# Optimization experiments

Measured on AMD Instinct MI355X. Metric: run time of the kernel, lower is better.

Reference implementation:

```python
import jax, jax.numpy as jnp
import numpy as np

N_NODES = 100000
N_EDGES = 1600000
IN_DIM = 128
HID_DIM = 64
OUT_DIM = 128
EPS = 1e-5


def setup_inputs() -> dict:
    key = jax.random.key(0)
    ks = jax.random.split(key, 10)
    feat = jax.random.normal(ks[0], (N_NODES, IN_DIM), dtype=jnp.float32)
    src = jax.random.randint(ks[1], (N_EDGES,), 0, N_NODES)
    dst = jax.random.randint(ks[2], (N_EDGES,), 0, N_NODES)
    # learned params
    gamma = jnp.ones((IN_DIM,), jnp.float32)
    beta = jnp.zeros((IN_DIM,), jnp.float32)
    Wq = jax.random.normal(ks[3], (IN_DIM, HID_DIM), jnp.float32) * 0.05
    bq = jax.random.normal(ks[4], (HID_DIM,), jnp.float32) * 0.05
    Wk = jax.random.normal(ks[5], (IN_DIM, HID_DIM), jnp.float32) * 0.05
    Wv = jax.random.normal(ks[6], (IN_DIM, OUT_DIM), jnp.float32) * 0.05
    We = jax.random.normal(ks[7], (HID_DIM, 1), jnp.float32) * 0.05
    return {"feat": feat, "src": src, "dst": dst, "gamma": gamma, "beta": beta,
            "Wq": Wq, "bq": bq, "Wk": Wk, "Wv": Wv, "We": We}


def reference(feat, src, dst, gamma, beta, Wq, bq, Wk, Wv, We):
    # BatchNorm1d (training-mode batch stats, biased variance)
    mean = jnp.mean(feat, axis=0)
    var = jnp.mean((feat - mean) ** 2, axis=0)
    x = (feat - mean) * jax.lax.rsqrt(var + EPS) * gamma + beta
    # feat_drop = 0.0 -> identity
    q = x @ Wq + bq          # [N, H]
    k = x @ Wk               # [N, H]
    v = x @ Wv               # [N, O]
    # u_add_v: src-node q + dst-node k per edge, then sigmoid and fc_e -> scalar score
    e = jax.nn.sigmoid(q[src] + k[dst]) @ We  # [E, 1]
    e = e[:, 0]                               # [E]
    # edge_softmax: softmax over incoming edges of each destination node
    m = jax.ops.segment_max(e, dst, num_segments=N_NODES)  # [N]
    ex = jnp.exp(e - m[dst])
    s = jax.ops.segment_sum(ex, dst, num_segments=N_NODES)  # [N]
    a = ex / s[dst]                                          # [E]
    # u_mul_e_sum: weighted scatter-sum of source v into destinations
    rst = jax.ops.segment_sum(v[src] * a[:, None], dst, num_segments=N_NODES)  # [N, O]
    return rst
```

## Files before the change

kernel.cpp:

```cpp
#include <hip/hip_runtime.h>
#include <math.h>

#define IN_DIM 128
#define HID 64
#define OUT_DIM 128
#define ELL_W 64
#define NPART 8
constexpr float EPS = 1e-5f;

typedef short short8 __attribute__((ext_vector_type(8)));
typedef float f32x4  __attribute__((ext_vector_type(4)));
typedef int   i32x4  __attribute__((ext_vector_type(4)));


__device__ inline ushort f2bf(float x) {
    __bf16 h = (__bf16)x;
    return *reinterpret_cast<ushort*>(&h);
}
__device__ inline short f2bfs(float x) {
    __bf16 h = (__bf16)x;
    return *reinterpret_cast<short*>(&h);
}
__device__ inline float bf2f(ushort u) {
    union { unsigned u; float f; } c; c.u = ((unsigned)u) << 16;
    return c.f;
}
__device__ inline float4 bf4_to_f4(ushort4 u) {
    return make_float4(bf2f(u.x), bf2f(u.y), bf2f(u.z), bf2f(u.w));
}

__global__ __launch_bounds__(256) void stats_kernel(
    const float* __restrict__ feat, float* __restrict__ ws, int n_nodes)
{
    int col  = threadIdx.x & 127;
    int half = threadIdx.x >> 7;
    float sum = 0.f, sq = 0.f;
    for (int r = blockIdx.x * 2 + half; r < n_nodes; r += gridDim.x * 2) {
        float x = feat[r * IN_DIM + col];
        sum += x; sq += x * x;
    }
    __shared__ float redS[256], redQ[256];
    redS[threadIdx.x] = sum; redQ[threadIdx.x] = sq;
    __syncthreads();
    if (threadIdx.x < 128) {
        sum = redS[threadIdx.x] + redS[threadIdx.x + 128];
        sq  = redQ[threadIdx.x] + redQ[threadIdx.x + 128];
        unsafeAtomicAdd(&ws[col], sum);
        unsafeAtomicAdd(&ws[128 + col], sq);
    }
}

__global__ __launch_bounds__(256) void wprep(
    const float* __restrict__ Wq, const float* __restrict__ Wk,
    const float* __restrict__ Wv, ushort* __restrict__ Bfrag)
{
    int gid  = blockIdx.x * 256 + threadIdx.x;
    int f    = gid >> 6;
    int lane = gid & 63;
    int kc = f & 3, ct = (f >> 2) & 3, w = f >> 4;
    int col   = w * 64 + ct * 16 + (lane & 15);
    int kbase = kc * 32 + (lane >> 4) * 8;
    ushort tmp[8];
    #pragma unroll
    for (int j = 0; j < 8; j++) {
        int k = kbase + j;
        float val;
        if (col < 64)       val = Wq[k * HID + col];
        else if (col < 128) val = Wk[k * HID + (col - 64)];
        else                val = Wv[k * OUT_DIM + (col - 128)];
        tmp[j] = f2bf(val);
    }
    ushort* d = &Bfrag[(f * 64 + lane) * 8];
    *(ushort4*)d       = make_ushort4(tmp[0], tmp[1], tmp[2], tmp[3]);
    *(ushort4*)(d + 4) = make_ushort4(tmp[4], tmp[5], tmp[6], tmp[7]);
}

__global__ __launch_bounds__(256) void mfma_qkv(
    const float* __restrict__ feat, const ushort* __restrict__ Bfrag,
    const float* __restrict__ bq,
    const float* __restrict__ gamma, const float* __restrict__ beta,
    const float* __restrict__ stats,
    ushort* __restrict__ qb, ushort* __restrict__ kb, ushort* __restrict__ vb,
    int n_nodes)
{
    __shared__ float sc[IN_DIM], sh[IN_DIM];
    int tid = threadIdx.x;
    if (tid < 128) {
        float inv_n = 1.0f / (float)n_nodes;
        float mean = stats[tid] * inv_n;
        float var  = stats[128 + tid] * inv_n - mean * mean;
        float s    = gamma[tid] * rsqrtf(var + EPS);
        sc[tid] = s; sh[tid] = beta[tid] - mean * s;
    }

    int w    = tid >> 6;
    int lane = tid & 63;
    int row0 = blockIdx.x * 64;
    int m    = lane & 15;
    int quad = lane >> 4;
    int nm1  = n_nodes - 1;

    short8 bfr[16];
    #pragma unroll
    for (int f = 0; f < 16; f++)
        bfr[f] = *(const short8*)&Bfrag[((w * 16 + f) * 64 + lane) * 8];

    __syncthreads();

    f32x4 acc[4][4] = {};

    #pragma unroll
    for (int kc = 0; kc < 4; kc++) {
        int koff = kc * 32 + quad * 8;
        float4 sc0 = *(const float4*)&sc[koff];
        float4 sc1 = *(const float4*)&sc[koff + 4];
        float4 sh0 = *(const float4*)&sh[koff];
        float4 sh1 = *(const float4*)&sh[koff + 4];
        short8 afr[4];
        #pragma unroll
        for (int rt = 0; rt < 4; rt++) {
            int row = row0 + rt * 16 + m;
            row = row < nm1 ? row : nm1;
            const float* fp = &feat[(size_t)row * IN_DIM + koff];
            float4 x0 = *(const float4*)fp;
            float4 x1 = *(const float4*)(fp + 4);
            afr[rt][0] = f2bfs(x0.x * sc0.x + sh0.x);
            afr[rt][1] = f2bfs(x0.y * sc0.y + sh0.y);
            afr[rt][2] = f2bfs(x0.z * sc0.z + sh0.z);
            afr[rt][3] = f2bfs(x0.w * sc0.w + sh0.w);
            afr[rt][4] = f2bfs(x1.x * sc1.x + sh1.x);
            afr[rt][5] = f2bfs(x1.y * sc1.y + sh1.y);
            afr[rt][6] = f2bfs(x1.z * sc1.z + sh1.z);
            afr[rt][7] = f2bfs(x1.w * sc1.w + sh1.w);
        }
        #pragma unroll
        for (int rt = 0; rt < 4; rt++)
            #pragma unroll
            for (int ct = 0; ct < 4; ct++)
                acc[rt][ct] = __builtin_amdgcn_mfma_f32_16x16x32_bf16(
                    afr[rt], bfr[ct * 4 + kc], acc[rt][ct], 0, 0, 0);
    }

    ushort* base; int ld, cl;
    if (w == 0)      { base = qb; ld = HID;     cl = 0; }
    else if (w == 1) { base = kb; ld = HID;     cl = 0; }
    else             { base = vb; ld = OUT_DIM; cl = (w - 2) * 64; }

    #pragma unroll
    for (int ct = 0; ct < 4; ct++) {
        int col = cl + ct * 16 + m;
        float bias = (w == 0) ? bq[ct * 16 + m] : 0.f;
        #pragma unroll
        for (int rt = 0; rt < 4; rt++) {
            int r0 = row0 + rt * 16 + quad * 4;
            #pragma unroll
            for (int r = 0; r < 4; r++)
                base[(size_t)(r0 + r) * ld + col] = f2bf(acc[rt][ct][r] + bias);
        }
    }
}

__global__ __launch_bounds__(256) void fill_ell_part(
    const int* __restrict__ src, const int* __restrict__ dst,
    int* __restrict__ deg, int* __restrict__ ell,
    int n_edges, int part_size)
{
    int p  = blockIdx.x & (NPART - 1);
    int gb = blockIdx.x >> 3;
    int nb = gridDim.x >> 3;
    unsigned lo = (unsigned)(p * part_size);
    unsigned ps = (unsigned)part_size;

    int idx    = gb * 256 + threadIdx.x;
    int stride = nb * 256;
    int n4     = n_edges >> 2;

    const i32x4* dst4 = reinterpret_cast<const i32x4*>(dst);
    const i32x4* src4 = reinterpret_cast<const i32x4*>(src);

    for (int i = idx; i < n4; i += stride) {
        i32x4 d4 = __builtin_nontemporal_load(dst4 + i);
        i32x4 s4 = __builtin_nontemporal_load(src4 + i);
        #pragma unroll
        for (int j = 0; j < 4; j++) {
            unsigned d = (unsigned)d4[j];
            if (d - lo < ps) {
                int pos = atomicAdd(&deg[d], 1);
                if (pos < ELL_W) ell[(size_t)d * ELL_W + pos] = s4[j];
            }
        }
    }
    for (int e = (n4 << 2) + idx; e < n_edges; e += stride) {
        unsigned d = (unsigned)dst[e];
        if (d - lo < ps) {
            int pos = atomicAdd(&deg[d], 1);
            if (pos < ELL_W) ell[(size_t)d * ELL_W + pos] = src[e];
        }
    }
}

__global__ __launch_bounds__(256) void hist_kernel(
    const int* __restrict__ dst, int* __restrict__ deg, int n_edges)
{
    int e = blockIdx.x * 256 + threadIdx.x;
    if (e < n_edges) atomicAdd(&deg[dst[e]], 1);
}

#define SCAN_B 256

__global__ __launch_bounds__(256) void scan_partial(
    const int* __restrict__ deg, int* __restrict__ part, int n)
{
    int chunk = (n + SCAN_B - 1) / SCAN_B;
    int lo = blockIdx.x * chunk;
    int hi = lo + chunk; if (hi > n) hi = n;
    int s = 0;
    for (int i = lo + threadIdx.x; i < hi; i += 256) s += deg[i];
    __shared__ int red[256];
    red[threadIdx.x] = s; __syncthreads();
    for (int d = 128; d; d >>= 1) {
        if (threadIdx.x < d) red[threadIdx.x] += red[threadIdx.x + d];
        __syncthreads();
    }
    if (threadIdx.x == 0) part[blockIdx.x] = red[0];
}

__global__ __launch_bounds__(256) void scan_combine(
    int* __restrict__ part, int* __restrict__ offsets, int n)
{
    __shared__ int tmp[256];
    int t = threadIdx.x;
    int v = part[t];
    tmp[t] = v; __syncthreads();
    for (int d = 1; d < 256; d <<= 1) {
        int cur = tmp[t];
        int add = (t >= d) ? tmp[t - d] : 0;
        __syncthreads();
        tmp[t] = cur + add;
        __syncthreads();
    }
    part[t] = tmp[t] - v;
    if (t == 255) offsets[n] = tmp[255];
}

__global__ __launch_bounds__(256) void scan_final(
    const int* __restrict__ deg, const int* __restrict__ part,
    int* __restrict__ offsets, int* __restrict__ cursor, int n)
{
    __shared__ int tmp[256];
    int t = threadIdx.x;
    int chunk = (n + SCAN_B - 1) / SCAN_B;
    int lo = blockIdx.x * chunk;
    int hi = lo + chunk; if (hi > n) hi = n;
    int base = part[blockIdx.x];
    for (int i0 = lo; i0 < hi; i0 += 256) {
        int i = i0 + t;
        int d = (i < hi) ? deg[i] : 0;
        tmp[t] = d; __syncthreads();
        for (int s = 1; s < 256; s <<= 1) {
            int cur = tmp[t];
            int add = (t >= s) ? tmp[t - s] : 0;
            __syncthreads();
            tmp[t] = cur + add;
            __syncthreads();
        }
        int excl = tmp[t] - d;
        int total = tmp[255];
        if (i < hi) { offsets[i] = base + excl; cursor[i] = base + excl; }
        base += total;
        __syncthreads();
    }
}

__global__ __launch_bounds__(256) void fill_kernel(
    const int* __restrict__ src, const int* __restrict__ dst,
    int* __restrict__ cursor, int* __restrict__ csr_src, int n_edges)
{
    int e = blockIdx.x * 256 + threadIdx.x;
    if (e < n_edges) {
        int d = dst[e];
        int pos = atomicAdd(&cursor[d], 1);
        csr_src[pos] = src[e];
    }
}

__device__ inline void gather_core(
    const int* __restrict__ row, int cnt, int node, int h, int sub,
    const ushort* __restrict__ qb, const ushort* __restrict__ kb,
    const ushort* __restrict__ vb, const float* __restrict__ We,
    float* __restrict__ out)
{
    if (cnt == 0) {
        if (sub == 0) {
            float4 z = make_float4(0.f, 0.f, 0.f, 0.f);
            *(float4*)&out[node * OUT_DIM + 4 * h]      = z;
            *(float4*)&out[node * OUT_DIM + 64 + 4 * h] = z;
        }
        return;
    }

    float4 kd = bf4_to_f4(*(const ushort4*)&kb[node * HID + 4 * h]);
    float4 we = *(const float4*)&We[4 * h];

    float4 o0 = make_float4(0.f, 0.f, 0.f, 0.f);
    float4 o1 = make_float4(0.f, 0.f, 0.f, 0.f);
    float ssum = 0.f;

    for (int p0 = 0; p0 < cnt; p0 += 4) {
        int p = p0 + sub;
        bool act = (p < cnt);
        int sN = row[act ? p : 0];
        float4 qv = bf4_to_f4(*(const ushort4*)&qb[sN * HID + 4 * h]);
        float t;
        t  = we.x * __fdividef(1.f, 1.f + __expf(-(qv.x + kd.x)));
        t += we.y * __fdividef(1.f, 1.f + __expf(-(qv.y + kd.y)));
        t += we.z * __fdividef(1.f, 1.f + __expf(-(qv.z + kd.z)));
        t += we.w * __fdividef(1.f, 1.f + __expf(-(qv.w + kd.w)));
        t += __shfl_xor(t, 1);
        t += __shfl_xor(t, 2);
        t += __shfl_xor(t, 4);
        t += __shfl_xor(t, 8);
        float exv = act ? __expf(t) : 0.f;
        ssum += exv;
        float4 v0 = bf4_to_f4(*(const ushort4*)&vb[sN * OUT_DIM + 4 * h]);
        float4 v1 = bf4_to_f4(*(const ushort4*)&vb[sN * OUT_DIM + 64 + 4 * h]);
        o0.x += exv * v0.x; o0.y += exv * v0.y;
        o0.z += exv * v0.z; o0.w += exv * v0.w;
        o1.x += exv * v1.x; o1.y += exv * v1.y;
        o1.z += exv * v1.z; o1.w += exv * v1.w;
    }

    ssum += __shfl_xor(ssum, 16); ssum += __shfl_xor(ssum, 32);
    o0.x += __shfl_xor(o0.x, 16); o0.x += __shfl_xor(o0.x, 32);
    o0.y += __shfl_xor(o0.y, 16); o0.y += __shfl_xor(o0.y, 32);
    o0.z += __shfl_xor(o0.z, 16); o0.z += __shfl_xor(o0.z, 32);
    o0.w += __shfl_xor(o0.w, 16); o0.w += __shfl_xor(o0.w, 32);
    o1.x += __shfl_xor(o1.x, 16); o1.x += __shfl_xor(o1.x, 32);
    o1.y += __shfl_xor(o1.y, 16); o1.y += __shfl_xor(o1.y, 32);
    o1.z += __shfl_xor(o1.z, 16); o1.z += __shfl_xor(o1.z, 32);
    o1.w += __shfl_xor(o1.w, 16); o1.w += __shfl_xor(o1.w, 32);

    if (sub == 0) {
        float inv = (ssum > 0.f) ? __fdividef(1.f, ssum) : 0.f;
        o0.x *= inv; o0.y *= inv; o0.z *= inv; o0.w *= inv;
        o1.x *= inv; o1.y *= inv; o1.z *= inv; o1.w *= inv;
        *(float4*)&out[node * OUT_DIM + 4 * h]      = o0;
        *(float4*)&out[node * OUT_DIM + 64 + 4 * h] = o1;
    }
}

__global__ __launch_bounds__(256) void gather_ell(
    const int* __restrict__ deg, const int* __restrict__ ell,
    const ushort* __restrict__ qb, const ushort* __restrict__ kb,
    const ushort* __restrict__ vb, const float* __restrict__ We,
    float* __restrict__ out, int n_nodes)
{
    int node = (blockIdx.x * 256 + threadIdx.x) >> 6;
    int lane = threadIdx.x & 63;
    if (node >= n_nodes) return;
    int cnt = deg[node];
    cnt = cnt < ELL_W ? cnt : ELL_W;
    gather_core(&ell[(size_t)node * ELL_W], cnt, node,
                lane & 15, lane >> 4, qb, kb, vb, We, out);
}

__global__ __launch_bounds__(256) void gather_csr(
    const int* __restrict__ offsets, const int* __restrict__ csr_src,
    const ushort* __restrict__ qb, const ushort* __restrict__ kb,
    const ushort* __restrict__ vb, const float* __restrict__ We,
    float* __restrict__ out, int n_nodes)
{
    int node = (blockIdx.x * 256 + threadIdx.x) >> 6;
    int lane = threadIdx.x & 63;
    if (node >= n_nodes) return;
    int beg = offsets[node];
    int cnt = offsets[node + 1] - beg;
    gather_core(&csr_src[beg], cnt, node,
                lane & 15, lane >> 4, qb, kb, vb, We, out);
}

extern "C" void kernel_launch(void* const* d_in, const int* in_sizes, int n_in,
                              void* d_out, int out_size, void* d_ws, size_t ws_size,
                              hipStream_t stream)
{
    const float* feat  = (const float*)d_in[0];
    const int*   src   = (const int*)d_in[1];
    const int*   dst   = (const int*)d_in[2];
    const float* gamma = (const float*)d_in[3];
    const float* beta  = (const float*)d_in[4];
    const float* Wq    = (const float*)d_in[5];
    const float* bq    = (const float*)d_in[6];
    const float* Wk    = (const float*)d_in[7];
    const float* Wv    = (const float*)d_in[8];
    const float* We    = (const float*)d_in[9];

    int n_nodes = in_sizes[0] / IN_DIM;
    int n_edges = in_sizes[1];
    int n_pad   = n_nodes + 64;
    size_t bfelems = (size_t)n_pad * (HID + HID + OUT_DIM) + 64 * 64 * 8;

    float* ws = (float*)d_ws;

    size_t ell_floats = 256 + (size_t)n_nodes * (1 + ELL_W) + 4;
    size_t ell_need   = (ell_floats + (bfelems + 1) / 2) * 4;

    int eb = (n_edges + 255) / 256;

    if (ws_size >= ell_need) {
        int* deg = (int*)(ws + 256);
        int* ell = deg + n_nodes;
        size_t off = 256 + (size_t)n_nodes * (1 + ELL_W);
        off = (off + 3) & ~(size_t)3;
        ushort* qb    = (ushort*)(ws + off);
        ushort* kb    = qb + (size_t)n_pad * HID;
        ushort* vb    = kb + (size_t)n_pad * HID;
        ushort* Bfrag = vb + (size_t)n_pad * OUT_DIM;

        int part_size = (n_nodes + NPART - 1) / NPART;

        hipMemsetAsync(ws, 0, (256 + (size_t)n_nodes) * sizeof(float), stream);
        stats_kernel<<<256, 256, 0, stream>>>(feat, ws, n_nodes);
        wprep<<<16, 256, 0, stream>>>(Wq, Wk, Wv, Bfrag);
        fill_ell_part<<<2048, 256, 0, stream>>>(
            src, dst, deg, ell, n_edges, part_size);
        mfma_qkv<<<(n_nodes + 63) / 64, 256, 0, stream>>>(
            feat, Bfrag, bq, gamma, beta, ws, qb, kb, vb, n_nodes);
        long long g_threads = (long long)n_nodes * 64;
        gather_ell<<<(int)((g_threads + 255) / 256), 256, 0, stream>>>(
            deg, ell, qb, kb, vb, We, (float*)d_out, n_nodes);
    } else {
        int* deg     = (int*)(ws + 256);
        int* offsets = deg + n_nodes;
        int* cursor  = offsets + n_nodes + 1;
        int* part    = cursor + n_nodes;
        int* csr_src = part + SCAN_B;
        size_t off = 256 + 3 * (size_t)n_nodes + 1 + SCAN_B + (size_t)n_edges;
        off = (off + 3) & ~(size_t)3;
        ushort* qb    = (ushort*)(ws + off);
        ushort* kb    = qb + (size_t)n_pad * HID;
        ushort* vb    = kb + (size_t)n_pad * HID;
        ushort* Bfrag = vb + (size_t)n_pad * OUT_DIM;

        hipMemsetAsync(ws, 0, (256 + (size_t)n_nodes) * sizeof(float), stream);
        stats_kernel<<<256, 256, 0, stream>>>(feat, ws, n_nodes);
        wprep<<<16, 256, 0, stream>>>(Wq, Wk, Wv, Bfrag);
        hist_kernel<<<eb, 256, 0, stream>>>(dst, deg, n_edges);
        scan_partial<<<SCAN_B, 256, 0, stream>>>(deg, part, n_nodes);
        scan_combine<<<1, 256, 0, stream>>>(part, offsets, n_nodes);
        scan_final<<<SCAN_B, 256, 0, stream>>>(deg, part, offsets, cursor, n_nodes);
        fill_kernel<<<eb, 256, 0, stream>>>(src, dst, cursor, csr_src, n_edges);
        mfma_qkv<<<(n_nodes + 63) / 64, 256, 0, stream>>>(
            feat, Bfrag, bq, gamma, beta, ws, qb, kb, vb, n_nodes);
        long long g_threads = (long long)n_nodes * 64;
        gather_csr<<<(int)((g_threads + 255) / 256), 256, 0, stream>>>(
            offsets, csr_src, qb, kb, vb, We, (float*)d_out, n_nodes);
    }
}
```

Before: 408.8 us.

## Interleave q and v rows, widen gather lanes, use XCD-aware work-stealing ELL fill

Stores q and v together in one 192-wide bf16 row per node, so each gathered source node is read from a single contiguous row. The gather now gives each lane 8 hidden and 16 output elements, with 8 edges processed in parallel per wavefront. The ELL build replaces static partition-by-block with per-XCD partitions, read via the XCC_ID hardware register, plus atomic chunked work stealing across partitions, aiming to keep the deg atomics local to each die's L2. This adds more registers per lane and depends on the XCD id register and a work-counter protocol.

```diff
diff --git a/kernel.cpp b/kernel.cpp
--- a/kernel.cpp
+++ b/kernel.cpp
@@ -24,9 +24,6 @@
 __device__ inline float bf2f(ushort u) {
     union { unsigned u; float f; } c; c.u = ((unsigned)u) << 16;
     return c.f;
-}
-__device__ inline float4 bf4_to_f4(ushort4 u) {
-    return make_float4(bf2f(u.x), bf2f(u.y), bf2f(u.z), bf2f(u.w));
 }
 
 __global__ __launch_bounds__(256) void stats_kernel(
@@ -80,7 +77,7 @@
     const float* __restrict__ bq,
     const float* __restrict__ gamma, const float* __restrict__ beta,
     const float* __restrict__ stats,
-    ushort* __restrict__ qb, ushort* __restrict__ kb, ushort* __restrict__ vb,
+    ushort* __restrict__ qvb, ushort* __restrict__ kb,
     int n_nodes)
 {
     __shared__ float sc[IN_DIM], sh[IN_DIM];
@@ -142,9 +139,8 @@
     }
 
     ushort* base; int ld, cl;
-    if (w == 0)      { base = qb; ld = HID;     cl = 0; }
-    else if (w == 1) { base = kb; ld = HID;     cl = 0; }
-    else             { base = vb; ld = OUT_DIM; cl = (w - 2) * 64; }
+    if (w == 1)      { base = kb;  ld = HID; cl = 0; }
+    else             { base = qvb; ld = 192; cl = (w == 0) ? 0 : 64 * (w - 1); }
 
     #pragma unroll
     for (int ct = 0; ct < 4; ct++) {
@@ -160,41 +156,55 @@
     }
 }
 
-__global__ __launch_bounds__(256) void fill_ell_part(
+__global__ __launch_bounds__(256) void fill_ell_xcd(
     const int* __restrict__ src, const int* __restrict__ dst,
-    int* __restrict__ deg, int* __restrict__ ell,
+    int* __restrict__ work, int* __restrict__ deg, int* __restrict__ ell,
     int n_edges, int part_size)
 {
-    int p  = blockIdx.x & (NPART - 1);
-    int gb = blockIdx.x >> 3;
-    int nb = gridDim.x >> 3;
-    unsigned lo = (unsigned)(p * part_size);
-    unsigned ps = (unsigned)part_size;
-
-    int idx    = gb * 256 + threadIdx.x;
-    int stride = nb * 256;
-    int n4     = n_edges >> 2;
-
+    int xcd;
+    asm volatile("s_getreg_b32 %0, hwreg(HW_REG_XCC_ID)" : "=s"(xcd));
+    xcd &= (NPART - 1);
+
+    int lane = threadIdx.x & 63;
+    const int CH = 2048;
+    int n4 = n_edges >> 2;
     const i32x4* dst4 = reinterpret_cast<const i32x4*>(dst);
     const i32x4* src4 = reinterpret_cast<const i32x4*>(src);
 
-    for (int i = idx; i < n4; i += stride) {
-        i32x4 d4 = __builtin_nontemporal_load(dst4 + i);
-        i32x4 s4 = __builtin_nontemporal_load(src4 + i);
-        #pragma unroll
-        for (int j = 0; j < 4; j++) {
-            unsigned d = (unsigned)d4[j];
-            if (d - lo < ps) {
-                int pos = atomicAdd(&deg[d], 1);
-                if (pos < ELL_W) ell[(size_t)d * ELL_W + pos] = s4[j];
+    for (int pi = 0; pi < NPART; ++pi) {
+        int p = (xcd + pi) & (NPART - 1);
+        unsigned lo = (unsigned)(p * part_size);
+        unsigned ps = (unsigned)part_size;
+        for (;;) {
+            if (*(volatile int*)&work[p] >= n_edges) break;
+            int base = 0;
+            if (lane == 0) base = atomicAdd(&work[p], CH);
+            base = __shfl(base, 0, 64);
+            if (base >= n_edges) break;
+
+            int i0 = base >> 2;
+            int i1 = (base + CH) >> 2; if (i1 > n4) i1 = n4;
+            for (int i = i0 + lane; i < i1; i += 64) {
+                i32x4 d4 = __builtin_nontemporal_load(dst4 + i);
+                i32x4 s4 = __builtin_nontemporal_load(src4 + i);
+                #pragma unroll
+                for (int j = 0; j < 4; j++) {
+                    unsigned d = (unsigned)d4[j];
+                    if (d - lo < ps) {
+                        int pos = atomicAdd(&deg[d], 1);
+                        if (pos < ELL_W) ell[(size_t)d * ELL_W + pos] = s4[j];
+                    }
+                }
             }
-        }
-    }
-    for (int e = (n4 << 2) + idx; e < n_edges; e += stride) {
-        unsigned d = (unsigned)dst[e];
-        if (d - lo < ps) {
-            int pos = atomicAdd(&deg[d], 1);
-            if (pos < ELL_W) ell[(size_t)d * ELL_W + pos] = src[e];
+            int t0 = base > (n4 << 2) ? base : (n4 << 2);
+            int t1 = base + CH; if (t1 > n_edges) t1 = n_edges;
+            for (int e = t0 + lane; e < t1; e += 64) {
+                unsigned d = (unsigned)dst[e];
+                if (d - lo < ps) {
+                    int pos = atomicAdd(&deg[d], 1);
+                    if (pos < ELL_W) ell[(size_t)d * ELL_W + pos] = src[e];
+                }
+            }
         }
     }
 }
@@ -286,73 +296,86 @@
 
 __device__ inline void gather_core(
     const int* __restrict__ row, int cnt, int node, int h, int sub,
-    const ushort* __restrict__ qb, const ushort* __restrict__ kb,
-    const ushort* __restrict__ vb, const float* __restrict__ We,
-    float* __restrict__ out)
-{
+    const ushort* __restrict__ qvb, const ushort* __restrict__ kb,
+    const float* __restrict__ We, float* __restrict__ out)
+{
+    int ob = node * OUT_DIM + 16 * h;
     if (cnt == 0) {
         if (sub == 0) {
             float4 z = make_float4(0.f, 0.f, 0.f, 0.f);
-            *(float4*)&out[node * OUT_DIM + 4 * h]      = z;
-            *(float4*)&out[node * OUT_DIM + 64 + 4 * h] = z;
+            #pragma unroll
+            for (int g = 0; g < 4; g++) *(float4*)&out[ob + 4 * g] = z;
         }
         return;
     }
 
-    float4 kd = bf4_to_f4(*(const ushort4*)&kb[node * HID + 4 * h]);
-    float4 we = *(const float4*)&We[4 * h];
-
-    float4 o0 = make_float4(0.f, 0.f, 0.f, 0.f);
-    float4 o1 = make_float4(0.f, 0.f, 0.f, 0.f);
+    float kd[8], we[8];
+    {
+        short8 k8 = *(const short8*)&kb[node * HID + 8 * h];
+        #pragma unroll
+        for (int j = 0; j < 8; j++) kd[j] = bf2f((ushort)k8[j]);
+        float4 wa = *(const float4*)&We[8 * h];
+        float4 wb = *(const float4*)&We[8 * h + 4];
+        we[0] = wa.x; we[1] = wa.y; we[2] = wa.z; we[3] = wa.w;
+        we[4] = wb.x; we[5] = wb.y; we[6] = wb.z; we[7] = wb.w;
+    }
+
+    float o[16];
+    #pragma unroll
+    for (int j = 0; j < 16; j++) o[j] = 0.f;
     float ssum = 0.f;
 
-    for (int p0 = 0; p0 < cnt; p0 += 4) {
+    for (int p0 = 0; p0 < cnt; p0 += 8) {
         int p = p0 + sub;
         bool act = (p < cnt);
         int sN = row[act ? p : 0];
-        float4 qv = bf4_to_f4(*(const ushort4*)&qb[sN * HID + 4 * h]);
-        float t;
-        t  = we.x * __fdividef(1.f, 1.f + __expf(-(qv.x + kd.x)));
-        t += we.y * __fdividef(1.f, 1.f + __expf(-(qv.y + kd.y)));
-        t += we.z * __fdividef(1.f, 1.f + __expf(-(qv.z + kd.z)));
-        t += we.w * __fdividef(1.f, 1.f + __expf(-(qv.w + kd.w)));
+        const ushort* qv = qvb + (size_t)sN * 192;
+
+        short8 q8 = *(const short8*)(qv + 8 * h);
+        float t = 0.f;
+        #pragma unroll
+        for (int j = 0; j < 8; j++) {
+            float x = bf2f((ushort)q8[j]) + kd[j];
+            t += we[j] * __fdividef(1.f, 1.f + __expf(-x));
+        }
         t += __shfl_xor(t, 1);
         t += __shfl_xor(t, 2);
         t += __shfl_xor(t, 4);
-        t += __shfl_xor(t, 8);
+
         float exv = act ? __expf(t) : 0.f;
         ssum += exv;
-        float4 v0 = bf4_to_f4(*(const ushort4*)&vb[sN * OUT_DIM + 4 * h]);
-        float4 v1 = bf4_to_f4(*(const ushort4*)&vb[sN * OUT_DIM + 64 + 4 * h]);
-        o0.x += exv * v0.x; o0.y += exv * v0.y;
-        o0.z += exv * v0.z; o0.w += exv * v0.w;
-        o1.x += exv * v1.x; o1.y += exv * v1.y;
-        o1.z += exv * v1.z; o1.w += exv * v1.w;
-    }
-
-    ssum += __shfl_xor(ssum, 16); ssum += __shfl_xor(ssum, 32);
-    o0.x += __shfl_xor(o0.x, 16); o0.x += __shfl_xor(o0.x, 32);
-    o0.y += __shfl_xor(o0.y, 16); o0.y += __shfl_xor(o0.y, 32);
-    o0.z += __shfl_xor(o0.z, 16); o0.z += __shfl_xor(o0.z, 32);
-    o0.w += __shfl_xor(o0.w, 16); o0.w += __shfl_xor(o0.w, 32);
-    o1.x += __shfl_xor(o1.x, 16); o1.x += __shfl_xor(o1.x, 32);
-    o1.y += __shfl_xor(o1.y, 16); o1.y += __shfl_xor(o1.y, 32);
-    o1.z += __shfl_xor(o1.z, 16); o1.z += __shfl_xor(o1.z, 32);
-    o1.w += __shfl_xor(o1.w, 16); o1.w += __shfl_xor(o1.w, 32);
+
+        short8 v0 = *(const short8*)(qv + 64 + 16 * h);
+        short8 v1 = *(const short8*)(qv + 72 + 16 * h);
+        #pragma unroll
+        for (int j = 0; j < 8; j++) {
+            o[j]     += exv * bf2f((ushort)v0[j]);
+            o[8 + j] += exv * bf2f((ushort)v1[j]);
+        }
+    }
+
+    #pragma unroll
+    for (int mm = 8; mm <= 32; mm <<= 1) {
+        ssum += __shfl_xor(ssum, mm);
+        #pragma unroll
+        for (int j = 0; j < 16; j++) o[j] += __shfl_xor(o[j], mm);
+    }
 
     if (sub == 0) {
         float inv = (ssum > 0.f) ? __fdividef(1.f, ssum) : 0.f;
-        o0.x *= inv; o0.y *= inv; o0.z *= inv; o0.w *= inv;
-        o1.x *= inv; o1.y *= inv; o1.z *= inv; o1.w *= inv;
-        *(float4*)&out[node * OUT_DIM + 4 * h]      = o0;
-        *(float4*)&out[node * OUT_DIM + 64 + 4 * h] = o1;
+        #pragma unroll
+        for (int g = 0; g < 4; g++) {
+            float4 r = make_float4(o[4 * g] * inv, o[4 * g + 1] * inv,
+                                   o[4 * g + 2] * inv, o[4 * g + 3] * inv);
+            *(float4*)&out[ob + 4 * g] = r;
+        }
     }
 }
 
 __global__ __launch_bounds__(256) void gather_ell(
     const int* __restrict__ deg, const int* __restrict__ ell,
-    const ushort* __restrict__ qb, const ushort* __restrict__ kb,
-    const ushort* __restrict__ vb, const float* __restrict__ We,
+    const ushort* __restrict__ qvb, const ushort* __restrict__ kb,
+    const float* __restrict__ We,
     float* __restrict__ out, int n_nodes)
 {
     int node = (blockIdx.x * 256 + threadIdx.x) >> 6;
@@ -361,13 +384,13 @@
     int cnt = deg[node];
     cnt = cnt < ELL_W ? cnt : ELL_W;
     gather_core(&ell[(size_t)node * ELL_W], cnt, node,
-                lane & 15, lane >> 4, qb, kb, vb, We, out);
+                lane & 7, lane >> 3, qvb, kb, We, out);
 }
 
 __global__ __launch_bounds__(256) void gather_csr(
     const int* __restrict__ offsets, const int* __restrict__ csr_src,
-    const ushort* __restrict__ qb, const ushort* __restrict__ kb,
-    const ushort* __restrict__ vb, const float* __restrict__ We,
+    const ushort* __restrict__ qvb, const ushort* __restrict__ kb,
+    const float* __restrict__ We,
     float* __restrict__ out, int n_nodes)
 {
     int node = (blockIdx.x * 256 + threadIdx.x) >> 6;
@@ -376,7 +399,7 @@
     int beg = offsets[node];
     int cnt = offsets[node + 1] - beg;
     gather_core(&csr_src[beg], cnt, node,
-                lane & 15, lane >> 4, qb, kb, vb, We, out);
+                lane & 7, lane >> 3, qvb, kb, We, out);
 }
 
 extern "C" void kernel_launch(void* const* d_in, const int* in_sizes, int n_in,
@@ -397,37 +420,37 @@
     int n_nodes = in_sizes[0] / IN_DIM;
     int n_edges = in_sizes[1];
     int n_pad   = n_nodes + 64;
-    size_t bfelems = (size_t)n_pad * (HID + HID + OUT_DIM) + 64 * 64 * 8;
+    size_t bfelems = (size_t)n_pad * (192 + HID) + 64 * 64 * 8;
 
     float* ws = (float*)d_ws;
 
-    size_t ell_floats = 256 + (size_t)n_nodes * (1 + ELL_W) + 4;
+    size_t ell_floats = 264 + (size_t)n_nodes * (1 + ELL_W) + 4;
     size_t ell_need   = (ell_floats + (bfelems + 1) / 2) * 4;
 
     int eb = (n_edges + 255) / 256;
 
     if (ws_size >= ell_need) {
-        int* deg = (int*)(ws + 256);
-        int* ell = deg + n_nodes;
-        size_t off = 256 + (size_t)n_nodes * (1 + ELL_W);
+        int* work = (int*)(ws + 256);
+        int* deg  = work + NPART;
+        int* ell  = deg + n_nodes;
+        size_t off = 264 + (size_t)n_nodes * (1 + ELL_W);
         off = (off + 3) & ~(size_t)3;
-        ushort* qb    = (ushort*)(ws + off);
-        ushort* kb    = qb + (size_t)n_pad * HID;
-        ushort* vb    = kb + (size_t)n_pad * HID;
-        ushort* Bfrag = vb + (size_t)n_pad * OUT_DIM;
+        ushort* qvb   = (ushort*)(ws + off);
+        ushort* kb    = qvb + (size_t)n_pad * 192;
+        ushort* Bfrag = kb + (size_t)n_pad * HID;
 
         int part_size = (n_nodes + NPART - 1) / NPART;
 
-        hipMemsetAsync(ws, 0, (256 + (size_t)n_nodes) * sizeof(float), stream);
+        hipMemsetAsync(ws, 0, (264 + (size_t)n_nodes) * sizeof(float), stream);
         stats_kernel<<<256, 256, 0, stream>>>(feat, ws, n_nodes);
         wprep<<<16, 256, 0, stream>>>(Wq, Wk, Wv, Bfrag);
-        fill_ell_part<<<2048, 256, 0, stream>>>(
-            src, dst, deg, ell, n_edges, part_size);
+        fill_ell_xcd<<<1024, 256, 0, stream>>>(
+            src, dst, work, deg, ell, n_edges, part_size);
         mfma_qkv<<<(n_nodes + 63) / 64, 256, 0, stream>>>(
-            feat, Bfrag, bq, gamma, beta, ws, qb, kb, vb, n_nodes);
+            feat, Bfrag, bq, gamma, beta, ws, qvb, kb, n_nodes);
         long long g_threads = (long long)n_nodes * 64;
         gather_ell<<<(int)((g_threads + 255) / 256), 256, 0, stream>>>(
-            deg, ell, qb, kb, vb, We, (float*)d_out, n_nodes);
+            deg, ell, qvb, kb, We, (float*)d_out, n_nodes);
     } else {
         int* deg     = (int*)(ws + 256);
         int* offsets = deg + n_nodes;
@@ -436,10 +459,9 @@
         int* csr_src = part + SCAN_B;
         size_t off = 256 + 3 * (size_t)n_nodes + 1 + SCAN_B + (size_t)n_edges;
         off = (off + 3) & ~(size_t)3;
-        ushort* qb    = (ushort*)(ws + off);
-        ushort* kb    = qb + (size_t)n_pad * HID;
-        ushort* vb    = kb + (size_t)n_pad * HID;
-        ushort* Bfrag = vb + (size_t)n_pad * OUT_DIM;
+        ushort* qvb   = (ushort*)(ws + off);
+        ushort* kb    = qvb + (size_t)n_pad * 192;
+        ushort* Bfrag = kb + (size_t)n_pad * HID;
 
         hipMemsetAsync(ws, 0, (256 + (size_t)n_nodes) * sizeof(float), stream);
         stats_kernel<<<256, 256, 0, stream>>>(feat, ws, n_nodes);
@@ -450,9 +472,9 @@
         scan_final<<<SCAN_B, 256, 0, stream>>>(deg, part, offsets, cursor, n_nodes);
         fill_kernel<<<eb, 256, 0, stream>>>(src, dst, cursor, csr_src, n_edges);
         mfma_qkv<<<(n_nodes + 63) / 64, 256, 0, stream>>>(
-            feat, Bfrag, bq, gamma, beta, ws, qb, kb, vb, n_nodes);
+            feat, Bfrag, bq, gamma, beta, ws, qvb, kb, n_nodes);
         long long g_threads = (long long)n_nodes * 64;
         gather_csr<<<(int)((g_threads + 255) / 256), 256, 0, stream>>>(
-            offsets, csr_src, qb, kb, vb, We, (float*)d_out, n_nodes);
-    }
-}
+            offsets, csr_src, qvb, kb, We, (float*)d_out, n_nodes);
+    }
+}
```

Result: slower. 639.5 us (+56.4%).
